# Performance work log

Hardware: AMD Instinct MI355X
Metric: run time of the kernel (lower is better)

The kernel has to match this reference:

```python
import jax, jax.numpy as jnp
import numpy as np
from jax import lax

B, NX, NY, NF = 4, 256, 256, 5
K, WIDTH, L = 4, 64, 4
MX, MY = 64, 64
NPARAMS, TSOFT, ODIM = 8, 10.0, 10

def gelu(v):
    return jax.nn.gelu(v, approximate=False)  # torch F.gelu default (erf)

def _dst(z):
    # DST via odd extension + rfft along axis -2 (Dirichlet BC in x)
    M = z.shape[-2]
    ext = jnp.concatenate([z, -jnp.flip(z[..., 1:M - 1, :], axis=-2)], axis=-2)  # len 2(M-1)
    return jnp.fft.rfft(ext, axis=-2, norm='ortho')  # M complex coeffs

def _idst(Z, M):
    ext = jnp.fft.irfft(Z, n=2 * (M - 1), axis=-2, norm='ortho')
    return ext[..., :M, :]

def setup_inputs() -> dict:
    key = jax.random.key(0)
    ks = iter(jax.random.split(key, 40))
    def rn(shape, s=0.05):
        return jax.random.normal(next(ks), shape, dtype=jnp.float32) * s
    return {
        'x': rn((B, NX, NY, NF), 1.0),
        'params': rn((B, NPARAMS), 1.0),
        'in_w': rn((NF + 2, WIDTH)), 'in_b': rn((WIDTH,)),
        'fnu_w1': rn((L, NPARAMS, 128)), 'fnu_b1': rn((L, 128)),
        'fnu_w2': rn((L, 128, 128)), 'fnu_b2': rn((L, 128)),
        'fnu_w3': rn((L, 128, K)), 'fnu_b3': rn((L, K)),
        'fw_y': rn((L, K, WIDTH, WIDTH, MY, 2)),
        'fw_x': rn((L, K, WIDTH, WIDTH, MX, 2)),
        'ff_w0': rn((L, WIDTH, 4 * WIDTH)), 'ff_b0': rn((L, 4 * WIDTH)),
        'ff_w1': rn((L, 4 * WIDTH, WIDTH)), 'ff_b1': rn((L, WIDTH)),
        'ln_g': jnp.ones((L, WIDTH), jnp.float32), 'ln_b': jnp.zeros((L, WIDTH), jnp.float32),
        'fa_w': rn((NF, WIDTH, 4 * ODIM - 4)), 'fa_b': rn((NF, 4 * ODIM - 4)),
        'fb_w': rn((NF, WIDTH, 34)), 'fb_b': rn((NF, 34)),
        'c1_w': rn((NF, 8, 1, 12)), 'c1_b': rn((NF, 8)),
        'c2_w': rn((NF, 1, 8, 12)), 'c2_b': rn((NF, 1)),
    }

def _forward(x, params, in_w, in_b, fnu_w1, fnu_b1, fnu_w2, fnu_b2, fnu_w3, fnu_b3,
             fw_y, fw_x, ff_w0, ff_b0, ff_w1, ff_b1, ln_g, ln_b,
             fa_w, fa_b, fb_w, fb_b, c1_w, c1_b, c2_w, c2_b):
    Bx, Nx, Ny, _ = x.shape
    x0 = x
    # normalized grid in [0, 2pi)
    gx = jnp.linspace(0.0, 2 * np.pi * (1 - 1.0 / Nx), Nx, dtype=jnp.float32)
    gy = jnp.linspace(0.0, 2 * np.pi * (1 - 1.0 / Ny), Ny, dtype=jnp.float32)
    grid = jnp.stack(jnp.broadcast_arrays(gx[:, None], gy[None, :]), axis=-1)  # (Nx,Ny,2)
    h = jnp.concatenate([x, jnp.broadcast_to(grid[None], (Bx, Nx, Ny, 2))], axis=-1)
    h = gelu(h @ in_w + in_b)  # (B,Nx,Ny,W)
    b = h
    for i in range(fw_y.shape[0]):
        # per-batch routing coefficients
        a = gelu(params @ fnu_w1[i] + fnu_b1[i])
        a = gelu(a @ fnu_w2[i] + fnu_b2[i])
        att = jax.nn.softmax((a @ fnu_w3[i] + fnu_b3[i]) / TSOFT, axis=-1)  # (B,K)
        z = h.transpose(0, 3, 1, 2)  # (B,I,M,N)
        attc = att.astype(jnp.complex64)
        wy = jnp.einsum('bk,kiom->biom', attc, fw_y[i, ..., 0] + 1j * fw_y[i, ..., 1])
        wx = jnp.einsum('bk,kiom->biom', attc, fw_x[i, ..., 0] + 1j * fw_x[i, ..., 1])
        # periodic y direction: rfft, truncate modes, complex conv, zero-pad, irfft
        zf_y = jnp.fft.rfft(z, axis=-1, norm='ortho')  # (B,I,M,N//2+1)
        low_y = jnp.einsum('bixm,biom->boxm', zf_y[..., :MY], wy)
        out_y = jnp.pad(low_y, ((0, 0), (0, 0), (0, 0), (0, zf_y.shape[-1] - MY)))
        xy = jnp.fft.irfft(out_y, n=Ny, axis=-1, norm='ortho')
        # Dirichlet x direction: DST via odd extension
        zf_x = _dst(z)  # (B,I,M,N) complex
        low_x = jnp.einsum('bixn,biox->boxn', zf_x[:, :, :MX, :], wx)
        out_x = jnp.pad(low_x, ((0, 0), (0, 0), (0, zf_x.shape[-2] - MX), (0, 0)))
        xx = _idst(out_x, Nx)
        r = (xx + xy).transpose(0, 2, 3, 1)  # (B,M,N,O)
        # backcast FeedForward: Linear->ReLU->Linear->LayerNorm
        t = jax.nn.relu(r @ ff_w0[i] + ff_b0[i])
        t = t @ ff_w1[i] + ff_b1[i]
        mu = t.mean(-1, keepdims=True)
        var = ((t - mu) ** 2).mean(-1, keepdims=True)
        b = (t - mu) / jnp.sqrt(var + 1e-5) * ln_g[i] + ln_b[i]
        h = h + b
    h = gelu(b)  # matches original: gelu of last backcast
    dn = ('NCH', 'OIH', 'NCH')
    outs = []
    for f in range(fa_w.shape[0]):
        ha = gelu(jnp.concatenate([h @ fa_w[f] + fa_b[f], h @ fb_w[f] + fb_b[f]], axis=-1))  # (B,Nx,Ny,70)
        u = ha.reshape(-1, 1, ha.shape[-1])
        u = lax.conv_general_dilated(u, c1_w[f], (2,), 'VALID', dimension_numbers=dn) + c1_b[f][None, :, None]
        u = gelu(u)
        u = lax.conv_general_dilated(u, c2_w[f], (2,), 'VALID', dimension_numbers=dn) + c2_b[f][None, :, None]
        outs.append(u.reshape(Bx, Nx, Ny, -1))  # (B,Nx,Ny,ODIM)
    out = jnp.stack(outs, axis=-2)  # (B,Nx,Ny,NF,ODIM)
    Tn = out.shape[-1]
    dt = jnp.arange(1, Tn + 1, dtype=out.dtype) / Tn
    return x0[..., None] + out * dt


def reference(x, params, in_w, in_b, fnu_w1, fnu_b1, fnu_w2, fnu_b2, fnu_w3, fnu_b3,
              fw_y, fw_x, ff_w0, ff_b0, ff_w1, ff_b1, ln_g, ln_b,
              fa_w, fa_b, fb_w, fb_b, c1_w, c1_b, c2_w, c2_b):
    return _forward(x, params, in_w, in_b, fnu_w1, fnu_b1, fnu_w2, fnu_b2, fnu_w3, fnu_b3,
                    fw_y, fw_x, ff_w0, ff_b0, ff_w1, ff_b1, ln_g, ln_b,
                    fa_w, fa_b, fb_w, fb_b, c1_w, c1_b, c2_w, c2_b)
```

## Files before the change

### kernel.cpp

```cpp
#include <hip/hip_runtime.h>
#include <math.h>


typedef __attribute__((ext_vector_type(8))) short sh8;
typedef __attribute__((ext_vector_type(4))) float f4;

__device__ __forceinline__ float fast_rcp(float x) {
#if defined(__has_builtin)
#if __has_builtin(__builtin_amdgcn_rcpf)
    return __builtin_amdgcn_rcpf(x);
#else
    return 1.0f / x;
#endif
#else
    return 1.0f / x;
#endif
}

__device__ __forceinline__ float gelu_f(float v) {
    return 0.5f * v * (1.0f + erff(v * 0.70710678118654752f));
}
__device__ __forceinline__ float gelu_fast(float v) {
    float s = v * (1.5957691216f + 0.0713548162f * v * v);
    float e = __expf(-s);
    return v * fast_rcp(1.0f + e);
}
__device__ __forceinline__ unsigned short f2bf(float x) {
    unsigned int u = __float_as_uint(x);
    u += 0x7fffu + ((u >> 16) & 1u);
    return (unsigned short)(u >> 16);
}
__device__ __forceinline__ float bf2f(unsigned short h) {
    return __uint_as_float(((unsigned int)h) << 16);
}

__global__ __launch_bounds__(256) void k_front(
    const float* __restrict__ ff_w0, const float* __restrict__ ff_w1,
    const float* __restrict__ fa_w, const float* __restrict__ fb_w,
    const float* __restrict__ fa_b, const float* __restrict__ fb_b,
    const float* __restrict__ c1w, const float* __restrict__ c2w,
    unsigned short* __restrict__ tabBf,
    unsigned short* __restrict__ W0T, unsigned short* __restrict__ W1T,
    unsigned short* __restrict__ Wcat, float* __restrict__ bcat,
    unsigned int* __restrict__ c1p, unsigned int* __restrict__ c2p,
    const float* __restrict__ params,
    const float* __restrict__ w1, const float* __restrict__ b1,
    const float* __restrict__ w2, const float* __restrict__ b2,
    const float* __restrict__ w3, const float* __restrict__ b3,
    float* __restrict__ att,
    const float* __restrict__ xin,
    const float* __restrict__ inw, const float* __restrict__ inb,
    unsigned short* __restrict__ Hb)
{
    int bid = blockIdx.x;
    int tid = threadIdx.x;
    if (bid == 0) {
        __shared__ float A1[128], A2[128], LG[4];
        int j = tid;
        for (int lay = 0; lay < 4; ++lay) {
            for (int b = 0; b < 4; ++b) {
                if (j < 128) {
                    float s = b1[lay * 128 + j];
                    for (int p = 0; p < 8; ++p)
                        s += params[b * 8 + p] * w1[(lay * 8 + p) * 128 + j];
                    A1[j] = gelu_f(s);
                }
                __syncthreads();
                if (j < 128) {
                    float s = b2[lay * 128 + j];
                    for (int q = 0; q < 128; ++q) s += A1[q] * w2[(lay * 128 + q) * 128 + j];
                    A2[j] = gelu_f(s);
                }
                __syncthreads();
                if (j < 4) {
                    float tacc = b3[lay * 4 + j];
                    for (int q = 0; q < 128; ++q) tacc += A2[q] * w3[(lay * 128 + q) * 4 + j];
                    LG[j] = tacc * 0.1f;
                }
                __syncthreads();
                if (j == 0) {
                    float mx = fmaxf(fmaxf(LG[0], LG[1]), fmaxf(LG[2], LG[3]));
                    float e0 = expf(LG[0] - mx), e1 = expf(LG[1] - mx);
                    float e2 = expf(LG[2] - mx), e3 = expf(LG[3] - mx);
                    float inv = 1.0f / (e0 + e1 + e2 + e3);
                    att[lay * 16 + b * 4 + 0] = e0 * inv;
                    att[lay * 16 + b * 4 + 1] = e1 * inv;
                    att[lay * 16 + b * 4 + 2] = e2 * inv;
                    att[lay * 16 + b * 4 + 3] = e3 * inv;
                }
                __syncthreads();
            }
        }
        return;
    }
    if (bid <= 1128) {
        int idx = (bid - 1) * 256 + tid;
        if (idx < 131072) {
            int t = idx >> 15, r = idx & 32767;
            const double PI = 3.14159265358979323846;
            const double s510 = 1.0 / sqrt(510.0);
            double v = 0.0;
            if (t == 0) {
                int row = r >> 8, y = r & 255;
                int m = row >> 1, c = row & 1;
                double ang = 2.0 * PI * (double)(m * y) / 256.0;
                v = (c == 0 ? cos(ang) : -sin(ang)) / 16.0;
            } else if (t == 1) {
                int row = r >> 8, xx = r & 255;
                int k = row >> 1, c = row & 1;
                if (c == 0) {
                    v = 0.0;
                    if (xx == 0)   v = s510;
                    if (xx == 255) v = (k & 1) ? -s510 : s510;
                } else {
                    double ang = PI * (double)(k * xx) / 255.0;
                    v = -2.0 * s510 * sin(ang);
                }
            } else if (t == 2) {
                int y = r >> 7, row = r & 127;
                int m = row >> 1, c = row & 1;
                double ang = 2.0 * PI * (double)(m * y) / 256.0;
                if (c == 0) v = (m == 0 ? 1.0 : 2.0 * cos(ang)) / 16.0;
                else        v = (m == 0 ? 0.0 : -2.0 * sin(ang) / 16.0);
            } else {
                int xx = r >> 7, row = r & 127;
                int k = row >> 1, c = row & 1;
                double ang = PI * (double)(k * xx) / 255.0;
                if (c == 0) v = s510 * (k == 0 ? 1.0 : 2.0 * cos(ang));
                else        v = (k == 0 ? 0.0 : -2.0 * s510 * sin(ang));
            }
            tabBf[idx] = f2bf((float)v);
            return;
        }
        idx -= 131072;
        if (idx < 65536) {
            int l = idx >> 14, rem = idx & 16383;
            int n = rem >> 6, k = rem & 63;
            W0T[idx] = f2bf(ff_w0[l * 16384 + k * 256 + n]);
        } else if (idx < 131072) {
            int j = idx - 65536;
            int l = j >> 14, rem = j & 16383;
            int n = rem >> 8, k = rem & 255;
            W1T[j] = f2bf(ff_w1[l * 16384 + k * 64 + n]);
        } else if (idx < 156672) {
            int j = idx - 131072;
            int f = j / 5120, r2 = j % 5120;
            int n = r2 >> 6, k = r2 & 63;
            float v = 0.0f;
            if (n < 36)      v = fa_w[f * 2304 + k * 36 + n];
            else if (n < 70) v = fb_w[f * 2176 + k * 34 + (n - 36)];
            Wcat[j] = f2bf(v);
        } else if (idx < 157072) {
            int j = idx - 156672;
            int f = j / 80, n = j % 80;
            float v = 0.0f;
            if (n < 36)      v = fa_b[f * 36 + n];
            else if (n < 70) v = fb_b[f * 34 + (n - 36)];
            bcat[j] = v;
        } else if (idx < 157552) {
            int j = idx - 157072;
            int half = j >= 240;
            int r = j - half * 240;
            int fc = r / 6, jj = r % 6;
            const float* src = half ? c2w : c1w;
            unsigned int u = (unsigned int)f2bf(src[fc * 12 + 2 * jj])
                           | ((unsigned int)f2bf(src[fc * 12 + 2 * jj + 1]) << 16);
            (half ? c2p : c1p)[r] = u;
        }
        return;
    }
    {
        long gid = (long)(bid - 1129) * 256 + tid;
        long px = gid >> 4;
        int c4 = (int)(gid & 15) * 4;
        int y = (int)(px & 255), xi = (int)((px >> 8) & 255);
        const float* xp = xin + px * 5;
        float v[7];
        v[0] = xp[0]; v[1] = xp[1]; v[2] = xp[2]; v[3] = xp[3]; v[4] = xp[4];
        const float STEP = 6.283185307179586f / 256.0f;
        v[5] = xi * STEP;
        v[6] = y * STEP;
        float r[4];
        #pragma unroll
        for (int c = 0; c < 4; ++c) {
            int ch = c4 + c;
            float s = inb[ch];
            #pragma unroll
            for (int p = 0; p < 7; ++p) s += v[p] * inw[p * 64 + ch];
            r[c] = gelu_fast(s);
        }
        uint2 uu;
        uu.x = (unsigned int)f2bf(r[0]) | ((unsigned int)f2bf(r[1]) << 16);
        uu.y = (unsigned int)f2bf(r[2]) | ((unsigned int)f2bf(r[3]) << 16);
        *(uint2*)(Hb + px * 64 + c4) = uu;
    }
}

__device__ __forceinline__ void stage_bt(unsigned short* lds, int pitch,
    const unsigned short* src, int rowStride, int K, int tid)
{
    int pairs = K >> 1;
    int tasks = pairs * 8;
    for (int idx = tid; idx < tasks; idx += 256) {
        int p = idx & (pairs - 1);
        int cg = idx / pairs;
        const unsigned short* s0 = src + (long)(2 * p) * rowStride + cg * 8;
        sh8 r0 = *(const sh8*)s0;
        sh8 r1 = *(const sh8*)(s0 + rowStride);
        unsigned short* dbase = lds + cg * 8 * pitch + 2 * p;
        #pragma unroll
        for (int j = 0; j < 8; ++j) {
            unsigned int u = (unsigned int)(unsigned short)r0[j]
                           | ((unsigned int)(unsigned short)r1[j] << 16);
            *(unsigned int*)(dbase + j * pitch) = u;
        }
    }
}

__global__ __launch_bounds__(256) void k_wtf(
    const float* __restrict__ fwY, const float* __restrict__ fwX,
    const float* __restrict__ att,
    unsigned short* __restrict__ WrTy, unsigned short* __restrict__ WiTy,
    unsigned short* __restrict__ WinTy,
    unsigned short* __restrict__ WrTx, unsigned short* __restrict__ WiTx,
    unsigned short* __restrict__ WinTx,
    const unsigned short* __restrict__ tabY, const unsigned short* __restrict__ tabX,
    const unsigned short* __restrict__ Hb,
    unsigned short* __restrict__ Zy, unsigned short* __restrict__ Zx)
{
    __shared__ __align__(16) unsigned char smem[34816];
    int bid = blockIdx.x;
    int tid = threadIdx.x;
    if (bid < 512) {
        int o = bid & 63, b = (bid >> 6) & 3, z = bid >> 8;
        const float* fw = z ? fwX : fwY;
        unsigned short* WrT  = z ? WrTx  : WrTy;
        unsigned short* WiT  = z ? WiTx  : WiTy;
        unsigned short* WinT = z ? WinTx : WinTy;
        float av[4];
        av[0] = att[b * 4 + 0]; av[1] = att[b * 4 + 1];
        av[2] = att[b * 4 + 2]; av[3] = att[b * 4 + 3];
        float acc[32];
        #pragma unroll
        for (int j = 0; j < 32; ++j) acc[j] = 0.0f;
        long toff = (long)(tid >> 7) * 8192 + o * 128 + (tid & 127);
        for (int k = 0; k < 4; ++k) {
            const float* p = fw + (long)k * 524288 + toff;
            float a = av[k];
            #pragma unroll
            for (int j = 0; j < 32; ++j) acc[j] += a * p[j * 16384];
        }
        float* ldsR = (float*)smem;
        float* ldsI = (float*)(smem + 16640);
        int m = (tid & 127) >> 1, c = tid & 1;
        int ib = tid >> 7;
        #pragma unroll
        for (int j = 0; j < 32; ++j) {
            int i = j * 2 + ib;
            (c ? ldsI : ldsR)[m * 65 + i] = acc[j];
        }
        __syncthreads();
        long ob = (long)b * 262144 + o * 64;
        #pragma unroll
        for (int it = 0; it < 16; ++it) {
            int idx = it * 256 + tid;
            int mm = idx >> 6, ii = idx & 63;
            float rr = ldsR[mm * 65 + ii], im = ldsI[mm * 65 + ii];
            long a = ob + (long)mm * 4096 + ii;
            WrT[a]  = f2bf(rr);
            WiT[a]  = f2bf(im);
            WinT[a] = f2bf(-im);
        }
        return;
    }
    unsigned short* ldsB = (unsigned short*)smem;
    int g2 = bid - 512;
    int br = g2 >> 10, g = g2 & 1023;
    int b = g >> 8, s = g & 255;
    const unsigned short* tab = br ? tabX : tabY;
    unsigned short* Zo = br ? Zx : Zy;
    long sLo = br ? 64L : 16384L;
    int rowStride = br ? 16384 : 64;
    const unsigned short* src = Hb + (long)b * 4194304 + (long)s * sLo;
    stage_bt(ldsB, 272, src, rowStride, 256, tid);
    __syncthreads();
    int w = tid >> 6, lane = tid & 63, q = lane >> 4, ln = lane & 15;
    f4 acc[2][4];
    #pragma unroll
    for (int mi = 0; mi < 2; ++mi)
        #pragma unroll
        for (int ni = 0; ni < 4; ++ni) acc[mi][ni] = (f4){0.f, 0.f, 0.f, 0.f};
    for (int kc = 0; kc < 256; kc += 32) {
        sh8 a[2], bf[4];
        #pragma unroll
        for (int mi = 0; mi < 2; ++mi)
            a[mi] = *(const sh8*)(tab + (w * 32 + mi * 16 + ln) * 256 + kc + q * 8);
        #pragma unroll
        for (int ni = 0; ni < 4; ++ni)
            bf[ni] = *(const sh8*)(ldsB + (ni * 16 + ln) * 272 + kc + q * 8);
        #pragma unroll
        for (int mi = 0; mi < 2; ++mi)
            #pragma unroll
            for (int ni = 0; ni < 4; ++ni)
                acc[mi][ni] = __builtin_amdgcn_mfma_f32_16x16x32_bf16(
                    a[mi], bf[ni], acc[mi][ni], 0, 0, 0);
    }
    long zB = (long)b * 2097152 + (long)s * 64;
    #pragma unroll
    for (int mi = 0; mi < 2; ++mi)
        #pragma unroll
        for (int ni = 0; ni < 4; ++ni)
            #pragma unroll
            for (int reg = 0; reg < 4; ++reg) {
                int r = w * 32 + mi * 16 + q * 4 + reg;
                Zo[zB + (long)r * 16384 + ni * 16 + ln] = f2bf(acc[mi][ni][reg]);
            }
}

__global__ __launch_bounds__(256) void k_mixm2(
    unsigned short* Zy, unsigned short* Zx,
    const unsigned short* __restrict__ WrTy, const unsigned short* __restrict__ WiTy,
    const unsigned short* __restrict__ WinTy,
    const unsigned short* __restrict__ WrTx, const unsigned short* __restrict__ WiTx,
    const unsigned short* __restrict__ WinTx)
{
    int xt = blockIdx.x, g = blockIdx.y, z = blockIdx.z;
    unsigned short* Z = z ? Zx : Zy;
    const unsigned short* WrT  = z ? WrTx  : WrTy;
    const unsigned short* WiT  = z ? WiTx  : WiTy;
    const unsigned short* WinT = z ? WinTx : WinTy;
    int b = g >> 6, m = g & 63;
    int tid = threadIdx.x, w = tid >> 6, lane = tid & 63, q = lane >> 4, ln = lane & 15;
    long zBr = (long)b * 2097152 + (long)(2 * m) * 16384;
    long wB = (long)b * 262144 + (long)m * 4096;
    int s0 = xt * 64 + w * 16;
    f4 aR[4], aI[4];
    #pragma unroll
    for (int nt = 0; nt < 4; ++nt) { aR[nt] = (f4){0.f,0.f,0.f,0.f}; aI[nt] = (f4){0.f,0.f,0.f,0.f}; }
    for (int kc = 0; kc < 64; kc += 32) {
        sh8 zr = *(const sh8*)(Z + zBr + (long)(s0 + ln) * 64 + kc + q * 8);
        sh8 zi = *(const sh8*)(Z + zBr + 16384 + (long)(s0 + ln) * 64 + kc + q * 8);
        #pragma unroll
        for (int nt = 0; nt < 4; ++nt) {
            int o = nt * 16 + ln;
            sh8 wr = *(const sh8*)(WrT + wB + o * 64 + kc + q * 8);
            sh8 wi = *(const sh8*)(WiT + wB + o * 64 + kc + q * 8);
            sh8 wn = *(const sh8*)(WinT + wB + o * 64 + kc + q * 8);
            aR[nt] = __builtin_amdgcn_mfma_f32_16x16x32_bf16(zr, wr, aR[nt], 0, 0, 0);
            aR[nt] = __builtin_amdgcn_mfma_f32_16x16x32_bf16(zi, wn, aR[nt], 0, 0, 0);
            aI[nt] = __builtin_amdgcn_mfma_f32_16x16x32_bf16(zr, wi, aI[nt], 0, 0, 0);
            aI[nt] = __builtin_amdgcn_mfma_f32_16x16x32_bf16(zi, wr, aI[nt], 0, 0, 0);
        }
    }
    #pragma unroll
    for (int nt = 0; nt < 4; ++nt)
        #pragma unroll
        for (int reg = 0; reg < 4; ++reg) {
            int s = s0 + q * 4 + reg;
            long a = zBr + (long)s * 64 + nt * 16 + ln;
            Z[a]          = f2bf(aR[nt][reg]);
            Z[a + 16384]  = f2bf(aI[nt][reg]);
        }
}

__global__ __launch_bounds__(256) void k_ti2(
    const unsigned short* __restrict__ tabY, const unsigned short* __restrict__ tabX,
    const unsigned short* __restrict__ Zy, const unsigned short* __restrict__ Zx,
    unsigned short* __restrict__ Ry, unsigned short* __restrict__ Rx)
{
    __shared__ __align__(16) unsigned short ldsB[64 * 144];
    int g = blockIdx.x, br = blockIdx.y;
    int b = g >> 8, s = g & 255;
    const unsigned short* tab = br ? tabX : tabY;
    const unsigned short* Zl  = br ? Zx : Zy;
    unsigned short* Ro = br ? Rx : Ry;
    int tid = threadIdx.x;
    const unsigned short* src = Zl + (long)b * 2097152 + (long)s * 64;
    stage_bt(ldsB, 144, src, 16384, 128, tid);
    __syncthreads();
    int w = tid >> 6, lane = tid & 63, q = lane >> 4, ln = lane & 15;
    f4 acc[4][4];
    #pragma unroll
    for (int mi = 0; mi < 4; ++mi)
        #pragma unroll
        for (int ni = 0; ni < 4; ++ni) acc[mi][ni] = (f4){0.f, 0.f, 0.f, 0.f};
    for (int kc = 0; kc < 128; kc += 32) {
        sh8 a[4], bf[4];
        #pragma unroll
        for (int mi = 0; mi < 4; ++mi)
            a[mi] = *(const sh8*)(tab + (w * 64 + mi * 16 + ln) * 128 + kc + q * 8);
        #pragma unroll
        for (int ni = 0; ni < 4; ++ni)
            bf[ni] = *(const sh8*)(ldsB + (ni * 16 + ln) * 144 + kc + q * 8);
        #pragma unroll
        for (int mi = 0; mi < 4; ++mi)
            #pragma unroll
            for (int ni = 0; ni < 4; ++ni)
                acc[mi][ni] = __builtin_amdgcn_mfma_f32_16x16x32_bf16(
                    a[mi], bf[ni], acc[mi][ni], 0, 0, 0);
    }
    long rB0 = (long)b * 4194304;
    #pragma unroll
    for (int mi = 0; mi < 4; ++mi)
        #pragma unroll
        for (int ni = 0; ni < 4; ++ni)
            #pragma unroll
            for (int reg = 0; reg < 4; ++reg) {
                int r2 = w * 64 + mi * 16 + q * 4 + reg;
                long a;
                if (br) a = rB0 + (long)r2 * 16384 + (long)s * 64 + ni * 16 + ln;
                else    a = rB0 + (long)s * 16384 + (long)r2 * 64 + ni * 16 + ln;
                Ro[a] = f2bf(acc[mi][ni][reg]);
            }
}

__global__ __launch_bounds__(256) void k_ffm(
    const unsigned short* __restrict__ Ry, const unsigned short* __restrict__ Rx,
    const unsigned short* __restrict__ W0T, const float* __restrict__ b0,
    const unsigned short* __restrict__ W1T, const float* __restrict__ b1,
    const float* __restrict__ g1, const float* __restrict__ be1,
    unsigned short* __restrict__ Hb, int last)
{
    __shared__ __align__(16) unsigned short T[64 * 264];
    int m0 = blockIdx.x * 64;
    int tid = threadIdx.x, w = tid >> 6, lane = tid & 63, q = lane >> 4, ln = lane & 15;
    int row = m0 + w * 16 + ln;
    const unsigned short* ryp = Ry + (long)row * 64;
    const unsigned short* rxp = Rx + (long)row * 64;
    float hbold[16];
    if (!last) {
        #pragma unroll
        for (int reg = 0; reg < 4; ++reg)
            #pragma unroll
            for (int nt = 0; nt < 4; ++nt)
                hbold[reg * 4 + nt] =
                    bf2f(Hb[(long)(m0 + w * 16 + q * 4 + reg) * 64 + nt * 16 + ln]);
    }
    {
        f4 acc1[16];
        #pragma unroll
        for (int nt = 0; nt < 16; ++nt) acc1[nt] = (f4){0.f, 0.f, 0.f, 0.f};
        for (int kc = 0; kc < 64; kc += 32) {
            sh8 ry = *(const sh8*)(ryp + kc + q * 8);
            sh8 rx = *(const sh8*)(rxp + kc + q * 8);
            sh8 a;
            #pragma unroll
            for (int j = 0; j < 8; ++j)
                a[j] = (short)f2bf(bf2f((unsigned short)ry[j]) + bf2f((unsigned short)rx[j]));
            #pragma unroll
            for (int nt = 0; nt < 16; ++nt) {
                sh8 bf = *(const sh8*)(W0T + (nt * 16 + ln) * 64 + kc + q * 8);
                acc1[nt] = __builtin_amdgcn_mfma_f32_16x16x32_bf16(a, bf, acc1[nt], 0, 0, 0);
            }
        }
        #pragma unroll
        for (int nt = 0; nt < 16; ++nt) {
            int n = nt * 16 + ln;
            float bias = b0[n];
            #pragma unroll
            for (int reg = 0; reg < 4; ++reg) {
                int m = w * 16 + q * 4 + reg;
                T[m * 264 + n] = f2bf(fmaxf(acc1[nt][reg] + bias, 0.0f));
            }
        }
    }
    f4 acc2[4];
    #pragma unroll
    for (int nt = 0; nt < 4; ++nt) acc2[nt] = (f4){0.f, 0.f, 0.f, 0.f};
    for (int kc = 0; kc < 256; kc += 32) {
        sh8 a = *(const sh8*)(T + (w * 16 + ln) * 264 + kc + q * 8);
        #pragma unroll
        for (int nt = 0; nt < 4; ++nt) {
            sh8 bf = *(const sh8*)(W1T + (nt * 16 + ln) * 256 + kc + q * 8);
            acc2[nt] = __builtin_amdgcn_mfma_f32_16x16x32_bf16(a, bf, acc2[nt], 0, 0, 0);
        }
    }
    float bia[4], gg[4], bb4[4];
    #pragma unroll
    for (int nt = 0; nt < 4; ++nt) {
        int n = nt * 16 + ln;
        bia[nt] = b1[n]; gg[nt] = g1[n]; bb4[nt] = be1[n];
    }
    #pragma unroll
    for (int reg = 0; reg < 4; ++reg) {
        float t[4];
        float s = 0.f, qs = 0.f;
        #pragma unroll
        for (int nt = 0; nt < 4; ++nt) {
            t[nt] = acc2[nt][reg] + bia[nt];
            s += t[nt]; qs += t[nt] * t[nt];
        }
        #pragma unroll
        for (int d = 1; d < 16; d <<= 1) {
            s  += __shfl_xor(s, d, 64);
            qs += __shfl_xor(qs, d, 64);
        }
        float mean = s * (1.0f / 64.0f);
        float var  = qs * (1.0f / 64.0f) - mean * mean;
        float inv  = rsqrtf(var + 1e-5f);
        int m = w * 16 + q * 4 + reg;
        long base = (long)(m0 + m) * 64;
        #pragma unroll
        for (int nt = 0; nt < 4; ++nt) {
            int n = nt * 16 + ln;
            float v = (t[nt] - mean) * inv * gg[nt] + bb4[nt];
            float hv;
            if (last) hv = gelu_fast(v);
            else      hv = hbold[reg * 4 + nt] + v;
            Hb[base + n] = f2bf(hv);
        }
    }
}

__global__ __launch_bounds__(256) void k_headm(
    const unsigned short* __restrict__ Hb, const float* __restrict__ x0,
    const unsigned short* __restrict__ Wcat, const float* __restrict__ bcat,
    const float* __restrict__ c1w, const float* __restrict__ c1b,
    const float* __restrict__ c2w, const float* __restrict__ c2b,
    float* __restrict__ out, int pxQ)
{
    __shared__ unsigned short ha[256 * 74];
    int tid = threadIdx.x;
    int f = blockIdx.y;
    long px0 = (long)(pxQ * 256 + blockIdx.x) * 256;
    int w = tid >> 6, lane = tid & 63, q = lane >> 4, ln = lane & 15;

    #pragma unroll
    for (int mi = 0; mi < 4; ++mi) {
        f4 acc[5];
        #pragma unroll
        for (int nt = 0; nt < 5; ++nt) acc[nt] = (f4){0.f, 0.f, 0.f, 0.f};
        #pragma unroll
        for (int kc = 0; kc < 2; ++kc) {
            sh8 a = *(const sh8*)(Hb + (px0 + w * 64 + mi * 16 + ln) * 64
                                   + kc * 32 + q * 8);
            #pragma unroll
            for (int nt = 0; nt < 5; ++nt) {
                sh8 bf = *(const sh8*)(Wcat + f * 5120 + (nt * 16 + ln) * 64
                                        + kc * 32 + q * 8);
                acc[nt] = __builtin_amdgcn_mfma_f32_16x16x32_bf16(a, bf, acc[nt], 0, 0, 0);
            }
        }
        #pragma unroll
        for (int nt = 0; nt < 5; ++nt) {
            int n = nt * 16 + ln;
            if (n < 70) {
                float bias = bcat[f * 80 + n];
                #pragma unroll
                for (int reg = 0; reg < 4; ++reg) {
                    int m = w * 64 + mi * 16 + q * 4 + reg;
                    ha[m * 74 + n] = f2bf(gelu_fast(acc[nt][reg] + bias));
                }
            }
        }
    }
    __syncthreads();

    float u2[10];
    float b2v = c2b[f];
    #pragma unroll
    for (int d = 0; d < 10; ++d) u2[d] = b2v;
    #pragma unroll
    for (int h = 0; h < 2; ++h) {
        float hw[40];
        #pragma unroll
        for (int i = 0; i < 20; ++i) {
            unsigned int u = *(const unsigned int*)(ha + tid * 74 + h * 30 + 2 * i);
            hw[2 * i]     = __uint_as_float(u << 16);
            hw[2 * i + 1] = __uint_as_float(u & 0xffff0000u);
        }
        #pragma unroll 1
        for (int c = 0; c < 8; ++c) {
            int fc = f * 8 + c;
            float w1r[12], w2r[12];
            #pragma unroll
            for (int j = 0; j < 12; ++j) {
                w1r[j] = c1w[fc * 12 + j];
                w2r[j] = c2w[fc * 12 + j];
            }
            float bc = c1b[fc];
            #pragma unroll
            for (int pl = 0; pl < 15; ++pl) {
                const int p = h * 15 + pl;
                float s = bc;
                #pragma unroll
                for (int j = 0; j < 12; ++j)
                    s = fmaf(hw[2 * pl + j], w1r[j], s);
                float g = gelu_fast(s);
                #pragma unroll
                for (int d = 0; d < 10; ++d) {
                    const int j2 = p - 2 * d;
                    if (j2 >= 0 && j2 < 12)
                        u2[d] = fmaf(g, w2r[j2], u2[d]);
                }
            }
        }
    }
    long px = px0 + tid;
    float xv = x0[px * 5 + f];
    #pragma unroll
    for (int d = 0; d < 10; ++d)
        out[px * 50 + f * 10 + d] = xv + u2[d] * (float)(d + 1) * 0.1f;
}

extern "C" void kernel_launch(void* const* d_in, const int* in_sizes, int n_in,
                              void* d_out, int out_size, void* d_ws, size_t ws_size,
                              hipStream_t stream) {
    (void)in_sizes; (void)n_in; (void)out_size; (void)ws_size;
    const float* xin    = (const float*)d_in[0];
    const float* params = (const float*)d_in[1];
    const float* in_w   = (const float*)d_in[2];
    const float* in_b   = (const float*)d_in[3];
    const float* fnu_w1 = (const float*)d_in[4];
    const float* fnu_b1 = (const float*)d_in[5];
    const float* fnu_w2 = (const float*)d_in[6];
    const float* fnu_b2 = (const float*)d_in[7];
    const float* fnu_w3 = (const float*)d_in[8];
    const float* fnu_b3 = (const float*)d_in[9];
    const float* fw_y   = (const float*)d_in[10];
    const float* fw_x   = (const float*)d_in[11];
    const float* ff_w0  = (const float*)d_in[12];
    const float* ff_b0  = (const float*)d_in[13];
    const float* ff_w1  = (const float*)d_in[14];
    const float* ff_b1  = (const float*)d_in[15];
    const float* ln_g   = (const float*)d_in[16];
    const float* ln_b   = (const float*)d_in[17];
    const float* fa_w   = (const float*)d_in[18];
    const float* fa_b   = (const float*)d_in[19];
    const float* fb_w   = (const float*)d_in[20];
    const float* fb_b   = (const float*)d_in[21];
    const float* c1_w   = (const float*)d_in[22];
    const float* c1_b   = (const float*)d_in[23];
    const float* c2_w   = (const float*)d_in[24];
    const float* c2_b   = (const float*)d_in[25];
    float* out = (float*)d_out;
    float* ws  = (float*)d_ws;

    unsigned short* tabBf = (unsigned short*)(ws + 0);
    unsigned short* tabYF = tabBf;
    unsigned short* tabXF = tabBf + 32768;
    unsigned short* tabYI = tabBf + 65536;
    unsigned short* tabXI = tabBf + 98304;
    unsigned short* W0T   = (unsigned short*)(ws + 65536);
    unsigned short* W1T   = (unsigned short*)(ws + 98304);
    unsigned short* Wcat  = (unsigned short*)(ws + 131072);
    float* bcat = ws + 143872;
    float* att  = ws + 144272;
    unsigned int* c1p = (unsigned int*)(ws + 144336);
    unsigned int* c2p = (unsigned int*)(ws + 144576);
    unsigned short* Hbf = (unsigned short*)(ws + 144816);
    unsigned short* WrTy  = (unsigned short*)(ws + 12727728);
    unsigned short* WiTy  = (unsigned short*)(ws + 13252016);
    unsigned short* WinTy = (unsigned short*)(ws + 13776304);
    unsigned short* WrTx  = (unsigned short*)(ws + 14300592);
    unsigned short* WiTx  = (unsigned short*)(ws + 14824880);
    unsigned short* WinTx = (unsigned short*)(ws + 15349168);
    unsigned short* Zy    = (unsigned short*)(ws + 15873456);
    unsigned short* Zx    = (unsigned short*)(ws + 20067760);
    unsigned short* Ry    = (unsigned short*)(ws + 24262064);
    unsigned short* Rx    = (unsigned short*)(ws + 32650672);

    k_front<<<17513, 256, 0, stream>>>(
        ff_w0, ff_w1, fa_w, fb_w, fa_b, fb_b, c1_w, c2_w,
        tabBf, W0T, W1T, Wcat, bcat, c1p, c2p,
        params, fnu_w1, fnu_b1, fnu_w2, fnu_b2, fnu_w3, fnu_b3, att,
        xin, in_w, in_b, Hbf);

    for (int lay = 0; lay < 4; ++lay) {
        const float* attL = att + lay * 16;
        k_wtf<<<2560, 256, 0, stream>>>(
            fw_y + (long)lay * 2097152, fw_x + (long)lay * 2097152, attL,
            WrTy, WiTy, WinTy, WrTx, WiTx, WinTx,
            tabYF, tabXF, Hbf, Zy, Zx);
        k_mixm2<<<dim3(4, 256, 2), 256, 0, stream>>>(
            Zy, Zx, WrTy, WiTy, WinTy, WrTx, WiTx, WinTx);
        k_ti2<<<dim3(1024, 2), 256, 0, stream>>>(tabYI, tabXI, Zy, Zx, Ry, Rx);
        k_ffm<<<4096, 256, 0, stream>>>(
            Ry, Rx, W0T + lay * 16384, ff_b0 + lay * 256,
            W1T + lay * 16384, ff_b1 + lay * 64,
            ln_g + lay * 64, ln_b + lay * 64,
            Hbf, (lay == 3) ? 1 : 0);
    }
    for (int pq = 0; pq < 4; ++pq)
        k_headm<<<dim3(256, 5), 256, 0, stream>>>(Hbf, xin, Wcat, bcat,
                                                  c1_w, c1_b, c2_w, c2_b, out, pq);
}
```

Before: 1.540 ms.

## Process four row tiles per k_ffm block with register prefetch of next tile

The FFN/LayerNorm kernel now has each block loop over four 64-row tiles, so the grid shrinks from 4096 to 1024 blocks. Before computing the current tile, it loads the next tile's Ry/Rx spectral outputs into registers. The intent is to hide global load latency and amortise per-block setup. The cost is extra registers for the prefetched data, which may lower occupancy, and fewer blocks available for latency hiding across the GPU.

Result: faster. 1.324 ms (-14.0%).

```diff
diff --git a/kernel.cpp b/kernel.cpp
--- a/kernel.cpp
+++ b/kernel.cpp
@@ -422,92 +422,112 @@
     unsigned short* __restrict__ Hb, int last)
 {
     __shared__ __align__(16) unsigned short T[64 * 264];
-    int m0 = blockIdx.x * 64;
     int tid = threadIdx.x, w = tid >> 6, lane = tid & 63, q = lane >> 4, ln = lane & 15;
-    int row = m0 + w * 16 + ln;
-    const unsigned short* ryp = Ry + (long)row * 64;
-    const unsigned short* rxp = Rx + (long)row * 64;
-    float hbold[16];
-    if (!last) {
-        #pragma unroll
-        for (int reg = 0; reg < 4; ++reg)
-            #pragma unroll
-            for (int nt = 0; nt < 4; ++nt)
-                hbold[reg * 4 + nt] =
-                    bf2f(Hb[(long)(m0 + w * 16 + q * 4 + reg) * 64 + nt * 16 + ln]);
-    }
+    int base0 = blockIdx.x * 256;
+    sh8 ryc[2], rxc[2];
     {
-        f4 acc1[16];
-        #pragma unroll
-        for (int nt = 0; nt < 16; ++nt) acc1[nt] = (f4){0.f, 0.f, 0.f, 0.f};
-        for (int kc = 0; kc < 64; kc += 32) {
-            sh8 ry = *(const sh8*)(ryp + kc + q * 8);
-            sh8 rx = *(const sh8*)(rxp + kc + q * 8);
-            sh8 a;
-            #pragma unroll
-            for (int j = 0; j < 8; ++j)
-                a[j] = (short)f2bf(bf2f((unsigned short)ry[j]) + bf2f((unsigned short)rx[j]));
+        long r0 = (long)(base0 + w * 16 + ln) * 64;
+        ryc[0] = *(const sh8*)(Ry + r0 + q * 8);
+        ryc[1] = *(const sh8*)(Ry + r0 + 32 + q * 8);
+        rxc[0] = *(const sh8*)(Rx + r0 + q * 8);
+        rxc[1] = *(const sh8*)(Rx + r0 + 32 + q * 8);
+    }
+    for (int it = 0; it < 4; ++it) {
+        int m0 = base0 + it * 64;
+        sh8 ryn[2], rxn[2];
+        if (it < 3) {
+            long rn = (long)(m0 + 64 + w * 16 + ln) * 64;
+            ryn[0] = *(const sh8*)(Ry + rn + q * 8);
+            ryn[1] = *(const sh8*)(Ry + rn + 32 + q * 8);
+            rxn[0] = *(const sh8*)(Rx + rn + q * 8);
+            rxn[1] = *(const sh8*)(Rx + rn + 32 + q * 8);
+        }
+        {
+            f4 acc1[16];
+            #pragma unroll
+            for (int nt = 0; nt < 16; ++nt) acc1[nt] = (f4){0.f, 0.f, 0.f, 0.f};
+            #pragma unroll
+            for (int kc2 = 0; kc2 < 2; ++kc2) {
+                sh8 a;
+                #pragma unroll
+                for (int j = 0; j < 8; ++j)
+                    a[j] = (short)f2bf(bf2f((unsigned short)ryc[kc2][j])
+                                     + bf2f((unsigned short)rxc[kc2][j]));
+                #pragma unroll
+                for (int nt = 0; nt < 16; ++nt) {
+                    sh8 bf = *(const sh8*)(W0T + (nt * 16 + ln) * 64 + kc2 * 32 + q * 8);
+                    acc1[nt] = __builtin_amdgcn_mfma_f32_16x16x32_bf16(a, bf, acc1[nt], 0, 0, 0);
+                }
+            }
             #pragma unroll
             for (int nt = 0; nt < 16; ++nt) {
-                sh8 bf = *(const sh8*)(W0T + (nt * 16 + ln) * 64 + kc + q * 8);
-                acc1[nt] = __builtin_amdgcn_mfma_f32_16x16x32_bf16(a, bf, acc1[nt], 0, 0, 0);
-            }
-        }
-        #pragma unroll
-        for (int nt = 0; nt < 16; ++nt) {
-            int n = nt * 16 + ln;
-            float bias = b0[n];
-            #pragma unroll
-            for (int reg = 0; reg < 4; ++reg) {
-                int m = w * 16 + q * 4 + reg;
-                T[m * 264 + n] = f2bf(fmaxf(acc1[nt][reg] + bias, 0.0f));
-            }
-        }
-    }
-    f4 acc2[4];
-    #pragma unroll
-    for (int nt = 0; nt < 4; ++nt) acc2[nt] = (f4){0.f, 0.f, 0.f, 0.f};
-    for (int kc = 0; kc < 256; kc += 32) {
-        sh8 a = *(const sh8*)(T + (w * 16 + ln) * 264 + kc + q * 8);
-        #pragma unroll
-        for (int nt = 0; nt < 4; ++nt) {
-            sh8 bf = *(const sh8*)(W1T + (nt * 16 + ln) * 256 + kc + q * 8);
-            acc2[nt] = __builtin_amdgcn_mfma_f32_16x16x32_bf16(a, bf, acc2[nt], 0, 0, 0);
-        }
-    }
-    float bia[4], gg[4], bb4[4];
-    #pragma unroll
-    for (int nt = 0; nt < 4; ++nt) {
-        int n = nt * 16 + ln;
-        bia[nt] = b1[n]; gg[nt] = g1[n]; bb4[nt] = be1[n];
-    }
-    #pragma unroll
-    for (int reg = 0; reg < 4; ++reg) {
-        float t[4];
-        float s = 0.f, qs = 0.f;
-        #pragma unroll
-        for (int nt = 0; nt < 4; ++nt) {
-            t[nt] = acc2[nt][reg] + bia[nt];
-            s += t[nt]; qs += t[nt] * t[nt];
-        }
-        #pragma unroll
-        for (int d = 1; d < 16; d <<= 1) {
-            s  += __shfl_xor(s, d, 64);
-            qs += __shfl_xor(qs, d, 64);
-        }
-        float mean = s * (1.0f / 64.0f);
-        float var  = qs * (1.0f / 64.0f) - mean * mean;
-        float inv  = rsqrtf(var + 1e-5f);
-        int m = w * 16 + q * 4 + reg;
-        long base = (long)(m0 + m) * 64;
+                int n = nt * 16 + ln;
+                float bias = b0[n];
+                #pragma unroll
+                for (int reg = 0; reg < 4; ++reg) {
+                    int m = w * 16 + q * 4 + reg;
+                    T[m * 264 + n] = f2bf(fmaxf(acc1[nt][reg] + bias, 0.0f));
+                }
+            }
+        }
+        float hbold[16];
+        if (!last) {
+            #pragma unroll
+            for (int reg = 0; reg < 4; ++reg)
+                #pragma unroll
+                for (int nt = 0; nt < 4; ++nt)
+                    hbold[reg * 4 + nt] =
+                        bf2f(Hb[(long)(m0 + w * 16 + q * 4 + reg) * 64 + nt * 16 + ln]);
+        }
+        f4 acc2[4];
+        #pragma unroll
+        for (int nt = 0; nt < 4; ++nt) acc2[nt] = (f4){0.f, 0.f, 0.f, 0.f};
+        for (int kc = 0; kc < 256; kc += 32) {
+            sh8 a = *(const sh8*)(T + (w * 16 + ln) * 264 + kc + q * 8);
+            #pragma unroll
+            for (int nt = 0; nt < 4; ++nt) {
+                sh8 bf = *(const sh8*)(W1T + (nt * 16 + ln) * 256 + kc + q * 8);
+                acc2[nt] = __builtin_amdgcn_mfma_f32_16x16x32_bf16(a, bf, acc2[nt], 0, 0, 0);
+            }
+        }
+        float bia[4], gg[4], bb4[4];
         #pragma unroll
         for (int nt = 0; nt < 4; ++nt) {
             int n = nt * 16 + ln;
-            float v = (t[nt] - mean) * inv * gg[nt] + bb4[nt];
-            float hv;
-            if (last) hv = gelu_fast(v);
-            else      hv = hbold[reg * 4 + nt] + v;
-            Hb[base + n] = f2bf(hv);
+            bia[nt] = b1[n]; gg[nt] = g1[n]; bb4[nt] = be1[n];
+        }
+        #pragma unroll
+        for (int reg = 0; reg < 4; ++reg) {
+            float t[4];
+            float s = 0.f, qs = 0.f;
+            #pragma unroll
+            for (int nt = 0; nt < 4; ++nt) {
+                t[nt] = acc2[nt][reg] + bia[nt];
+                s += t[nt]; qs += t[nt] * t[nt];
+            }
+            #pragma unroll
+            for (int d = 1; d < 16; d <<= 1) {
+                s  += __shfl_xor(s, d, 64);
+                qs += __shfl_xor(qs, d, 64);
+            }
+            float mean = s * (1.0f / 64.0f);
+            float var  = qs * (1.0f / 64.0f) - mean * mean;
+            float inv  = rsqrtf(var + 1e-5f);
+            int m = w * 16 + q * 4 + reg;
+            long base = (long)(m0 + m) * 64;
+            #pragma unroll
+            for (int nt = 0; nt < 4; ++nt) {
+                int n = nt * 16 + ln;
+                float v = (t[nt] - mean) * inv * gg[nt] + bb4[nt];
+                float hv;
+                if (last) hv = gelu_fast(v);
+                else      hv = hbold[reg * 4 + nt] + v;
+                Hb[base + n] = f2bf(hv);
+            }
+        }
+        if (it < 3) {
+            ryc[0] = ryn[0]; ryc[1] = ryn[1];
+            rxc[0] = rxn[0]; rxc[1] = rxn[1];
         }
     }
 }
@@ -675,7 +695,7 @@
         k_mixm2<<<dim3(4, 256, 2), 256, 0, stream>>>(
             Zy, Zx, WrTy, WiTy, WinTy, WrTx, WiTx, WinTx);
         k_ti2<<<dim3(1024, 2), 256, 0, stream>>>(tabYI, tabXI, Zy, Zx, Ry, Rx);
-        k_ffm<<<4096, 256, 0, stream>>>(
+        k_ffm<<<1024, 256, 0, stream>>>(
             Ry, Rx, W0T + lay * 16384, ff_b0 + lay * 256,
             W1T + lay * 16384, ff_b1 + lay * 64,
             ln_g + lay * 64, ln_b + lay * 64,
```
